# Kernel optimization log

Hardware: AMD Instinct MI355X
Metric: run time of the kernel (lower is better)

Reference implementation:

```python
import jax, jax.numpy as jnp
import numpy as np

N_NODES = 50000
N_EDGES = 1600000
IN_DIM = 128
HID = 64
HEADS = 4
N_GRAPHS = 64
OUT_DIM = 10
NEG_SLOPE = 0.2  # PyG GATConv default leaky_relu slope


def _glorot(key, shape):
    fan_in = shape[0] if len(shape) > 1 else shape[-1]
    return jax.random.normal(key, shape, dtype=jnp.float32) / np.sqrt(fan_in)


def setup_inputs() -> dict:
    key = jax.random.key(0)
    ks = jax.random.split(key, 24)
    imgs = jax.random.normal(ks[0], (N_NODES, IN_DIM), dtype=jnp.float32)
    edge_index = jax.random.randint(ks[1], (2, N_EDGES), 0, N_NODES, dtype=jnp.int32)
    batch = jnp.sort(jax.random.randint(ks[2], (N_NODES,), 0, N_GRAPHS, dtype=jnp.int32))
    HC = HID * HEADS
    inp = {
        'imgs': imgs, 'edge_index': edge_index, 'batch': batch,
        # superpixel aggregator: Linear(input_dim, hidden)
        'W_agg': _glorot(ks[3], (IN_DIM, HID)), 'b_agg': jnp.zeros((HID,), jnp.float32),
        # GAT layer 0: hidden -> heads*hidden, concat
        'W0': _glorot(ks[4], (HID, HC)), 'as0': _glorot(ks[5], (HEADS, HID)), 'ad0': _glorot(ks[6], (HEADS, HID)), 'b0': jnp.zeros((HC,), jnp.float32),
        # GAT layer 1: heads*hidden -> heads*hidden, concat
        'W1': _glorot(ks[7], (HC, HC)), 'as1': _glorot(ks[8], (HEADS, HID)), 'ad1': _glorot(ks[9], (HEADS, HID)), 'b1': jnp.zeros((HC,), jnp.float32),
        # GAT layer 2: heads*hidden -> hidden, mean over heads
        'W2': _glorot(ks[10], (HC, HC)), 'as2': _glorot(ks[11], (HEADS, HID)), 'ad2': _glorot(ks[12], (HEADS, HID)), 'b2': jnp.zeros((HID,), jnp.float32),
        # MLP: hidden -> hidden -> out
        'mW1': _glorot(ks[13], (HID, HID)), 'mb1': jnp.zeros((HID,), jnp.float32),
        'mW2': _glorot(ks[14], (HID, OUT_DIM)), 'mb2': jnp.zeros((OUT_DIM,), jnp.float32),
    }
    return inp


def _gat_conv(x, src, dst, W, a_src, a_dst, b, concat):
    # PyG GATConv: linear -> per-head scores -> leaky_relu -> segment softmax over dst -> scatter-add
    N = x.shape[0]
    H, C = a_src.shape
    h = (x @ W).reshape(N, H, C)                      # [N,H,C]
    es = jnp.sum(h * a_src, axis=-1)                  # [N,H]
    ed = jnp.sum(h * a_dst, axis=-1)                  # [N,H]
    e = jax.nn.leaky_relu(es[src] + ed[dst], NEG_SLOPE)  # [E,H]
    m = jax.ops.segment_max(e, dst, num_segments=N)
    m = jnp.where(jnp.isfinite(m), m, 0.0)
    ex = jnp.exp(e - m[dst])                          # [E,H]
    s = jax.ops.segment_sum(ex, dst, num_segments=N)
    alpha = ex / (s[dst] + 1e-16)                     # [E,H]
    out = jax.ops.segment_sum(h[src] * alpha[..., None], dst, num_segments=N)  # [N,H,C]
    out = out.reshape(N, H * C) if concat else out.mean(axis=1)
    return out + b


def _forward(imgs, edge_index, batch, W_agg, b_agg, W0, as0, ad0, b0, W1, as1, ad1, b1, W2, as2, ad2, b2, mW1, mb1, mW2, mb2):
    N = imgs.shape[0]
    # add self loops (PyG GATConv default add_self_loops=True)
    loop = jnp.arange(N, dtype=edge_index.dtype)
    src = jnp.concatenate([edge_index[0], loop])
    dst = jnp.concatenate([edge_index[1], loop])
    x = imgs @ W_agg + b_agg                          # lrgb aggregator
    x = jax.nn.elu(_gat_conv(x, src, dst, W0, as0, ad0, b0, True))
    x = jax.nn.elu(_gat_conv(x, src, dst, W1, as1, ad1, b1, True))
    x = _gat_conv(x, src, dst, W2, as2, ad2, b2, False)
    # global mean pool over graphs
    sums = jax.ops.segment_sum(x, batch, num_segments=N_GRAPHS)
    cnt = jax.ops.segment_sum(jnp.ones((N,), x.dtype), batch, num_segments=N_GRAPHS)
    pooled = sums / jnp.maximum(cnt, 1.0)[:, None]
    # MLP (dropout inactive at inference)
    hmlp = jax.nn.relu(pooled @ mW1 + mb1)
    return hmlp @ mW2 + mb2


def reference(imgs, edge_index, batch, W_agg, b_agg, W0, as0, ad0, b0, W1, as1, ad1, b1, W2, as2, ad2, b2, mW1, mb1, mW2, mb2):
    return _forward(imgs, edge_index, batch, W_agg, b_agg, W0, as0, ad0, b0, W1, as1, ad1, b1, W2, as2, ad2, b2, mW1, mb1, mW2, mb2)
```

## Files before the change

### kernel.cpp

```cpp
#include <hip/hip_runtime.h>
#include <hip/hip_bf16.h>

#define N_NODES 50000
#define N_EDGESX 1600000
#define E_TOT   (N_EDGESX + N_NODES)
#define IN_DIM 128
#define HID 64
#define HEADS 4
#define HC 256
#define N_GRAPHS 64
#define OUT_DIM 10
#define NEG_SLOPE 0.2f

#define NBUK 196
#define CAP 12288
#define BT 4096

typedef __attribute__((ext_vector_type(8))) short bf16x8;
typedef __attribute__((ext_vector_type(4))) float f32x4;

__device__ __forceinline__ float lrelu(float x){ return fmaxf(x, NEG_SLOPE*x); }
__device__ __forceinline__ float sel4(float4 v, int i){
  float r = v.x;
  r = (i==1) ? v.y : r;
  r = (i==2) ? v.z : r;
  r = (i==3) ? v.w : r;
  return r;
}
__device__ __forceinline__ unsigned short f2bf(float f){
  union { __hip_bfloat16 b; unsigned short u; } cv;
  cv.b = __float2bfloat16(f);
  return cv.u;
}
__device__ __forceinline__ float bflo(unsigned int u){ return __uint_as_float(u << 16); }
__device__ __forceinline__ float bfhi(unsigned int u){ return __uint_as_float(u & 0xffff0000u); }

__global__ __launch_bounds__(256) void bin_k(const int* __restrict__ ei,
                                             int* __restrict__ bucket_cursor,
                                             unsigned int* __restrict__ bucket_buf){
  __shared__ unsigned int pk[BT];
  __shared__ unsigned int binned[BT];
  __shared__ int hist[256], excl[256], gbase[256], lcur[256], tmp[256];
  const int tid = threadIdx.x;
  const int e0 = blockIdx.x * BT;
  const int nv = min(BT, E_TOT - e0);
  hist[tid] = 0;
  __syncthreads();
  for (int i = tid; i < nv; i += 256){
    int e = e0 + i;
    int src, dst;
    if (e < N_EDGESX){ src = ei[e]; dst = ei[N_EDGESX + e]; }
    else { src = e - N_EDGESX; dst = src; }
    pk[i] = ((unsigned)src << 16) | (unsigned)dst;
    atomicAdd(&hist[dst >> 8], 1);
  }
  __syncthreads();
  int v = hist[tid];
  tmp[tid] = v;
  __syncthreads();
  for (int off = 1; off < 256; off <<= 1){
    int t = (tid >= off) ? tmp[tid-off] : 0;
    __syncthreads();
    tmp[tid] += t;
    __syncthreads();
  }
  excl[tid] = tmp[tid] - v;
  lcur[tid] = tmp[tid] - v;
  if (tid < NBUK && v > 0) gbase[tid] = atomicAdd(&bucket_cursor[tid], v);
  __syncthreads();
  for (int i = tid; i < nv; i += 256){
    unsigned u = pk[i];
    int b = (int)((u & 0xFFFFu) >> 8);
    int p = atomicAdd(&lcur[b], 1);
    binned[p] = u;
  }
  __syncthreads();
  for (int j = tid; j < nv; j += 256){
    unsigned u = binned[j];
    int b = (int)((u & 0xFFFFu) >> 8);
    bucket_buf[(size_t)b*CAP + gbase[b] + (j - excl[b])] = u;
  }
}

__global__ __launch_bounds__(256) void bucket_scan_k(const int* __restrict__ bucket_cursor,
                                                     int* __restrict__ bucket_base,
                                                     int* __restrict__ row_start){
  __shared__ int tmp[256];
  int t = threadIdx.x;
  int v = (t < NBUK) ? bucket_cursor[t] : 0;
  tmp[t] = v;
  __syncthreads();
  for (int off = 1; off < 256; off <<= 1){
    int x = (t >= off) ? tmp[t-off] : 0;
    __syncthreads();
    tmp[t] += x;
    __syncthreads();
  }
  if (t < NBUK) bucket_base[t] = tmp[t] - v;
  if (t == 0) row_start[N_NODES] = E_TOT;
}

__global__ __launch_bounds__(256) void build_k(const unsigned int* __restrict__ bucket_buf,
                                               const int* __restrict__ bucket_cursor,
                                               const int* __restrict__ bucket_base,
                                               int* __restrict__ row_start,
                                               int* __restrict__ csr_src){
  __shared__ int hist[256], excl[256], lcur[256], tmp[256];
  const int b = blockIdx.x;
  const int t = threadIdx.x;
  const int cntb = bucket_cursor[b];
  const int base = bucket_base[b];
  const unsigned int* buf = bucket_buf + (size_t)b*CAP;
  hist[t] = 0;
  __syncthreads();
  for (int i = t; i < cntb; i += 256) atomicAdd(&hist[buf[i] & 255], 1);
  __syncthreads();
  int v = hist[t];
  tmp[t] = v;
  __syncthreads();
  for (int off = 1; off < 256; off <<= 1){
    int x = (t >= off) ? tmp[t-off] : 0;
    __syncthreads();
    tmp[t] += x;
    __syncthreads();
  }
  excl[t] = tmp[t] - v;
  lcur[t] = tmp[t] - v;
  int g = b*256 + t;
  if (g < N_NODES) row_start[g] = base + excl[t];
  __syncthreads();
  for (int i = t; i < cntb; i += 256){
    unsigned u = buf[i];
    int p = atomicAdd(&lcur[u & 255], 1);
    csr_src[base + p] = (int)(u >> 16);
  }
}

__global__ __launch_bounds__(256) void wcvt_k(const float* __restrict__ W, unsigned short* __restrict__ WT, int K){
  int idx = blockIdx.x*256 + threadIdx.x;
  if (idx >= K*256) return;
  int k = idx >> 8, c = idx & 255;
  WT[c*K + k] = f2bf(W[k*256 + c]);
}

__global__ __launch_bounds__(256) void agg_lin(const float* __restrict__ imgs, const float* __restrict__ W,
                                               const float* __restrict__ b, unsigned short* __restrict__ x0){
  __shared__ __align__(16) float xr[4][IN_DIM];
  int w = threadIdx.x >> 6, lane = threadIdx.x & 63;
  int n = blockIdx.x*4 + w;
  if (n >= N_NODES) return;
  ((float2*)xr[w])[lane] = ((const float2*)(imgs + (size_t)n*IN_DIM))[lane];
  float acc = b[lane];
  #pragma unroll 8
  for (int k = 0; k < IN_DIM; k++)
    acc = fmaf(xr[w][k], W[k*HID + lane], acc);
  x0[(size_t)n*HID + lane] = f2bf(acc);
}

template<int K>
__global__ __launch_bounds__(256) void lin_mfma(const unsigned short* __restrict__ x,
                                                const unsigned short* __restrict__ WT,
                                                const float* __restrict__ as_, const float* __restrict__ ad_,
                                                unsigned short* __restrict__ h,
                                                float* __restrict__ es, float* __restrict__ ed){
  constexpr int KP = K + 8;
  __shared__ __align__(16) unsigned short xs[16][KP];
  const int tid = threadIdx.x;
  const int lane = tid & 63;
  const int w = tid >> 6;
  const int n0 = blockIdx.x * 16;
  constexpr int CH = K/8;
  for (int i = tid; i < 16*CH; i += 256){
    int r = i / CH, cc = (i % CH)*8;
    *(uint4*)(&xs[r][cc]) = *(const uint4*)(x + (size_t)(n0+r)*K + cc);
  }
  __syncthreads();
  const int g  = lane >> 4;
  const int cl = lane & 15;
  f32x4 acc[4];
  #pragma unroll
  for (int c = 0; c < 4; c++) acc[c] = (f32x4){0.f,0.f,0.f,0.f};
  #pragma unroll
  for (int t = 0; t < K/32; t++){
    bf16x8 a = *(const bf16x8*)(&xs[cl][t*32 + g*8]);
    #pragma unroll
    for (int c = 0; c < 4; c++){
      bf16x8 bv = *(const bf16x8*)(WT + (size_t)(w*64 + c*16 + cl)*K + t*32 + g*8);
      acc[c] = __builtin_amdgcn_mfma_f32_16x16x32_bf16(a, bv, acc[c], 0, 0, 0);
    }
  }
  float pes[4] = {0.f,0.f,0.f,0.f}, ped[4] = {0.f,0.f,0.f,0.f};
  #pragma unroll
  for (int c = 0; c < 4; c++){
    float av = as_[w*64 + c*16 + cl];
    float dv = ad_[w*64 + c*16 + cl];
    #pragma unroll
    for (int j = 0; j < 4; j++){
      pes[j] = fmaf(acc[c][j], av, pes[j]);
      ped[j] = fmaf(acc[c][j], dv, ped[j]);
    }
  }
  #pragma unroll
  for (int off = 8; off >= 1; off >>= 1){
    #pragma unroll
    for (int j = 0; j < 4; j++){
      pes[j] += __shfl_xor(pes[j], off);
      ped[j] += __shfl_xor(ped[j], off);
    }
  }
  if (cl == 0){
    #pragma unroll
    for (int j = 0; j < 4; j++){
      int n = n0 + g*4 + j;
      es[n*4 + w] = pes[j];
      ed[n*4 + w] = ped[j];
    }
  }
  #pragma unroll
  for (int c = 0; c < 4; c++){
    #pragma unroll
    for (int j = 0; j < 4; j++){
      h[(size_t)(n0 + g*4 + j)*HC + w*64 + c*16 + cl] = f2bf(acc[c][j]);
    }
  }
}

template<int ACT, int OBF>
__global__ __launch_bounds__(256) void gat_agg(const unsigned short* __restrict__ h,
    const float* __restrict__ es, const float* __restrict__ ed,
    const int* __restrict__ row_start, const int* __restrict__ csr_src,
    const float* __restrict__ bias, void* __restrict__ outp){
  __shared__ int   sbuf[4][64];
  __shared__ float wbuf[4][64][4];
  const int lane = threadIdx.x & 63;
  const int wid  = threadIdx.x >> 6;
  const int n = blockIdx.x*4 + wid;
  if (n >= N_NODES) return;
  const int rs = row_start[n], re = row_start[n+1];
  const float4 edn = *(const float4*)(ed + n*4);
  const int half = lane >> 5;
  const int l5   = lane & 31;
  const int hh   = l5 >> 3;
  const unsigned voff_lane = (unsigned)(l5 << 3);

  float4 sum4 = make_float4(0.f,0.f,0.f,0.f);
  float a0=0.f,a1=0.f,a2=0.f,a3=0.f,a4=0.f,a5=0.f,a6=0.f,a7=0.f;

  for (int base = rs; base < re; base += 64){
    const int cl = min(64, re - base);
    int e = base + lane;
    int s = (e < re) ? csr_src[e] : 0;
    float4 e4 = *(const float4*)(es + (s<<2));
    float w0 = __expf(lrelu(e4.x + edn.x));
    float w1 = __expf(lrelu(e4.y + edn.y));
    float w2 = __expf(lrelu(e4.z + edn.z));
    float w3 = __expf(lrelu(e4.w + edn.w));
    if (e >= re){ w0=0.f; w1=0.f; w2=0.f; w3=0.f; }
    sum4.x += w0; sum4.y += w1; sum4.z += w2; sum4.w += w3;
    sbuf[wid][lane] = s;
    float4 wv4; wv4.x=w0; wv4.y=w1; wv4.z=w2; wv4.w=w3;
    *(float4*)wbuf[wid][lane] = wv4;
    for (int j = 0; j < cl; j += 2){
      int jj = j + half;
      float a  = wbuf[wid][jj][hh];
      int   s2 = sbuf[wid][jj];
      uint4 hv = *(const uint4*)(h + ((unsigned)(s2<<8) + voff_lane));
      a0 = fmaf(a, bflo(hv.x), a0);
      a1 = fmaf(a, bfhi(hv.x), a1);
      a2 = fmaf(a, bflo(hv.y), a2);
      a3 = fmaf(a, bfhi(hv.y), a3);
      a4 = fmaf(a, bflo(hv.z), a4);
      a5 = fmaf(a, bfhi(hv.z), a5);
      a6 = fmaf(a, bflo(hv.w), a6);
      a7 = fmaf(a, bfhi(hv.w), a7);
    }
  }
  #pragma unroll
  for (int off = 32; off >= 1; off >>= 1){
    sum4.x += __shfl_xor(sum4.x, off);
    sum4.y += __shfl_xor(sum4.y, off);
    sum4.z += __shfl_xor(sum4.z, off);
    sum4.w += __shfl_xor(sum4.w, off);
  }
  const float inv = 1.f / (sel4(sum4, hh) + 1e-16f);
  a0 += __shfl_xor(a0, 32); a1 += __shfl_xor(a1, 32);
  a2 += __shfl_xor(a2, 32); a3 += __shfl_xor(a3, 32);
  a4 += __shfl_xor(a4, 32); a5 += __shfl_xor(a5, 32);
  a6 += __shfl_xor(a6, 32); a7 += __shfl_xor(a7, 32);
  float4 o;
  o.x = (half ? a4 : a0) * inv;
  o.y = (half ? a5 : a1) * inv;
  o.z = (half ? a6 : a2) * inv;
  o.w = (half ? a7 : a3) * inv;
  const int fbase = l5*8 + half*4;
  if (ACT){
    float4 b4 = *(const float4*)(bias + fbase);
    o.x += b4.x; o.y += b4.y; o.z += b4.z; o.w += b4.w;
    o.x = o.x > 0.f ? o.x : expm1f(o.x);
    o.y = o.y > 0.f ? o.y : expm1f(o.y);
    o.z = o.z > 0.f ? o.z : expm1f(o.z);
    o.w = o.w > 0.f ? o.w : expm1f(o.w);
  }
  if (OBF){
    ushort4 ob;
    ob.x = f2bf(o.x); ob.y = f2bf(o.y); ob.z = f2bf(o.z); ob.w = f2bf(o.w);
    *(ushort4*)((unsigned short*)outp + (size_t)n*HC + fbase) = ob;
  } else {
    *(float4*)((float*)outp + (size_t)n*HC + fbase) = o;
  }
}

#define PB_NODES 128
__global__ __launch_bounds__(256) void pool_k(const float* __restrict__ xagg,
                                              const int* __restrict__ batch, float* __restrict__ pooled,
                                              float* __restrict__ cnt){
  int c = threadIdx.x & 63;
  int sub = threadIdx.x >> 6;
  int n0 = blockIdx.x * PB_NODES;
  int nend = n0 + PB_NODES; if (nend > N_NODES) nend = N_NODES;
  float acc = 0.f; int curg = -1; int cl = 0;
  for (int n = n0 + sub; n < nend; n += 4){
    int g = batch[n];
    if (g != curg){
      if (curg >= 0){
        unsafeAtomicAdd(pooled + curg*HID + c, acc);
        if (c == 0) unsafeAtomicAdd(cnt + curg, (float)cl);
      }
      curg = g; acc = 0.f; cl = 0;
    }
    const float* r = xagg + (size_t)n*HC;
    acc += 0.25f*(r[c] + r[64+c] + r[128+c] + r[192+c]);
    cl++;
  }
  if (curg >= 0){
    unsafeAtomicAdd(pooled + curg*HID + c, acc);
    if (c == 0) unsafeAtomicAdd(cnt + curg, (float)cl);
  }
}

__global__ __launch_bounds__(64) void mlp_k(const float* __restrict__ pooled, const float* __restrict__ cnt,
                                            const float* __restrict__ b2,
                                            const float* __restrict__ mW1, const float* __restrict__ mb1,
                                            const float* __restrict__ mW2, const float* __restrict__ mb2,
                                            float* __restrict__ out){
  __shared__ float p[HID], h1[HID];
  int g = blockIdx.x, j = threadIdx.x;
  float c = fmaxf(cnt[g], 1.f);
  p[j] = pooled[g*HID + j] / c + b2[j];
  __syncthreads();
  float acc = mb1[j];
  #pragma unroll 8
  for (int k = 0; k < HID; k++) acc = fmaf(p[k], mW1[k*HID + j], acc);
  h1[j] = fmaxf(acc, 0.f);
  __syncthreads();
  if (j < OUT_DIM){
    float a2 = mb2[j];
    #pragma unroll 8
    for (int k = 0; k < HID; k++) a2 = fmaf(h1[k], mW2[k*OUT_DIM + j], a2);
    out[g*OUT_DIM + j] = a2;
  }
}

extern "C" void kernel_launch(void* const* d_in, const int* in_sizes, int n_in,
                              void* d_out, int out_size, void* d_ws, size_t ws_size,
                              hipStream_t stream){
  const float* imgs  = (const float*)d_in[0];
  const int*   ei    = (const int*)d_in[1];
  const int*   batch = (const int*)d_in[2];
  const float* W_agg = (const float*)d_in[3];
  const float* b_agg = (const float*)d_in[4];
  const float* W0 = (const float*)d_in[5];
  const float* as0 = (const float*)d_in[6];
  const float* ad0 = (const float*)d_in[7];
  const float* b0 = (const float*)d_in[8];
  const float* W1 = (const float*)d_in[9];
  const float* as1 = (const float*)d_in[10];
  const float* ad1 = (const float*)d_in[11];
  const float* b1 = (const float*)d_in[12];
  const float* W2 = (const float*)d_in[13];
  const float* as2 = (const float*)d_in[14];
  const float* ad2 = (const float*)d_in[15];
  const float* b2 = (const float*)d_in[16];
  const float* mW1 = (const float*)d_in[17];
  const float* mb1 = (const float*)d_in[18];
  const float* mW2 = (const float*)d_in[19];
  const float* mb2 = (const float*)d_in[20];
  float* out = (float*)d_out;

  float* xf32 = (float*)d_ws;
  unsigned short* hb  = (unsigned short*)(xf32 + (size_t)N_NODES*HC);
  unsigned short* xbf = hb + (size_t)N_NODES*HC;
  float* es   = (float*)(xbf + (size_t)N_NODES*HC);
  float* ed   = es + (size_t)N_NODES*HEADS;
  float* pooled = ed + (size_t)N_NODES*HEADS;
  float* cnt  = pooled + N_GRAPHS*HID;
  int* row_start = (int*)(cnt + N_GRAPHS);
  int* csr_src   = row_start + (N_NODES+1);
  int* bucket_cursor = csr_src + E_TOT;
  int* bucket_base   = bucket_cursor + NBUK;
  unsigned short* WT0 = (unsigned short*)(bucket_base + NBUK);
  unsigned short* WT1 = WT0 + 256*64;
  unsigned short* WT2 = WT1 + 256*256;
  unsigned int* bucket_buf = (unsigned int*)(WT2 + 256*256);

  hipMemsetAsync(bucket_cursor, 0, NBUK*sizeof(int), stream);
  bin_k<<<(E_TOT + BT - 1)/BT, 256, 0, stream>>>(ei, bucket_cursor, bucket_buf);
  bucket_scan_k<<<1, 256, 0, stream>>>(bucket_cursor, bucket_base, row_start);
  build_k<<<NBUK, 256, 0, stream>>>(bucket_buf, bucket_cursor, bucket_base, row_start, csr_src);

  wcvt_k<<<(64*256+255)/256, 256, 0, stream>>>(W0, WT0, 64);
  wcvt_k<<<(256*256+255)/256, 256, 0, stream>>>(W1, WT1, 256);
  wcvt_k<<<(256*256+255)/256, 256, 0, stream>>>(W2, WT2, 256);

  agg_lin<<<(N_NODES+3)/4, 256, 0, stream>>>(imgs, W_agg, b_agg, xbf);

  const int MB = N_NODES/16;
  const int GB = (N_NODES + 3)/4;

  lin_mfma<64><<<MB, 256, 0, stream>>>(xbf, WT0, as0, ad0, hb, es, ed);
  gat_agg<1,1><<<GB, 256, 0, stream>>>(hb, es, ed, row_start, csr_src, b0, xbf);

  lin_mfma<256><<<MB, 256, 0, stream>>>(xbf, WT1, as1, ad1, hb, es, ed);
  gat_agg<1,1><<<GB, 256, 0, stream>>>(hb, es, ed, row_start, csr_src, b1, xbf);

  lin_mfma<256><<<MB, 256, 0, stream>>>(xbf, WT2, as2, ad2, hb, es, ed);
  gat_agg<0,0><<<GB, 256, 0, stream>>>(hb, es, ed, row_start, csr_src, nullptr, xf32);

  hipMemsetAsync(pooled, 0, (N_GRAPHS*HID + N_GRAPHS)*sizeof(float), stream);
  pool_k<<<(N_NODES + PB_NODES - 1)/PB_NODES, 256, 0, stream>>>(xf32, batch, pooled, cnt);
  mlp_k<<<N_GRAPHS, 64, 0, stream>>>(pooled, cnt, b2, mW1, mb1, mW2, mb2, out);
}
```

Measured before the change: 620.1 us.

## Aggregate before projecting in GAT layer 0 and split later aggregations per head

Layer 0 now computes attention scores straight from the 64-dim input through precomputed W0·a vectors. It aggregates the 64-dim features per head and only then applies the W0 projection, bias and ELU in a separate MFMA GEMM. This shrinks the per-edge gather from 256 to 64 bf16 values. Layers 1 and 2 store h in a head-major layout and launch one grid slice per head, which is meant to improve cache locality of the gathered rows, at the cost of recomputing the edge weights four times. Intermediate buffers reuse workspace regions such as bucket_buf and xf32.

```diff
diff --git a/kernel.cpp b/kernel.cpp
--- a/kernel.cpp
+++ b/kernel.cpp
@@ -143,8 +143,25 @@
   WT[c*K + k] = f2bf(W[k*256 + c]);
 }
 
+__global__ __launch_bounds__(256) void wproj_k(const float* __restrict__ W0,
+    const float* __restrict__ as0, const float* __restrict__ ad0,
+    float* __restrict__ ws0, float* __restrict__ wd0){
+  int t = threadIdx.x;
+  int h = t >> 6, k = t & 63;
+  float s = 0.f, d = 0.f;
+  for (int c = 0; c < 64; c++){
+    float wv = W0[k*256 + h*64 + c];
+    s = fmaf(wv, as0[h*64 + c], s);
+    d = fmaf(wv, ad0[h*64 + c], d);
+  }
+  ws0[t] = s; wd0[t] = d;
+}
+
 __global__ __launch_bounds__(256) void agg_lin(const float* __restrict__ imgs, const float* __restrict__ W,
-                                               const float* __restrict__ b, unsigned short* __restrict__ x0){
+                                               const float* __restrict__ b,
+                                               const float* __restrict__ ws0, const float* __restrict__ wd0,
+                                               unsigned short* __restrict__ x0,
+                                               float* __restrict__ es, float* __restrict__ ed){
   __shared__ __align__(16) float xr[4][IN_DIM];
   int w = threadIdx.x >> 6, lane = threadIdx.x & 63;
   int n = blockIdx.x*4 + w;
@@ -155,13 +172,150 @@
   for (int k = 0; k < IN_DIM; k++)
     acc = fmaf(xr[w][k], W[k*HID + lane], acc);
   x0[(size_t)n*HID + lane] = f2bf(acc);
+  float p[4], q[4];
+  #pragma unroll
+  for (int h = 0; h < 4; h++){
+    p[h] = acc * ws0[h*64 + lane];
+    q[h] = acc * wd0[h*64 + lane];
+  }
+  #pragma unroll
+  for (int off = 32; off >= 1; off >>= 1){
+    #pragma unroll
+    for (int h = 0; h < 4; h++){
+      p[h] += __shfl_xor(p[h], off);
+      q[h] += __shfl_xor(q[h], off);
+    }
+  }
+  if (lane == 0){
+    float4 pv; pv.x=p[0]; pv.y=p[1]; pv.z=p[2]; pv.w=p[3];
+    float4 qv; qv.x=q[0]; qv.y=q[1]; qv.z=q[2]; qv.w=q[3];
+    *(float4*)(es + n*4) = pv;
+    *(float4*)(ed + n*4) = qv;
+  }
+}
+
+__global__ __launch_bounds__(256) void gat_agg0(const unsigned short* __restrict__ x0,
+    const float* __restrict__ es, const float* __restrict__ ed,
+    const int* __restrict__ row_start, const int* __restrict__ csr_src,
+    unsigned short* __restrict__ y4){
+  __shared__ int   sbuf[4][64];
+  __shared__ float wbuf[4][64][4];
+  const int lane = threadIdx.x & 63;
+  const int wid  = threadIdx.x >> 6;
+  const int n = blockIdx.x*4 + wid;
+  if (n >= N_NODES) return;
+  const int rs = row_start[n], re = row_start[n+1];
+  const float4 edn = *(const float4*)(ed + n*4);
+  const int slot = lane >> 3;
+  const int f8   = lane & 7;
+  float4 sumw = make_float4(0.f,0.f,0.f,0.f);
+  float acc[4][8];
+  #pragma unroll
+  for (int h=0;h<4;h++)
+    #pragma unroll
+    for (int q2=0;q2<8;q2++) acc[h][q2]=0.f;
+
+  for (int base = rs; base < re; base += 64){
+    const int cl = min(64, re - base);
+    int e = base + lane;
+    int s = (e < re) ? csr_src[e] : 0;
+    float4 e4 = *(const float4*)(es + (s<<2));
+    float w0 = __expf(lrelu(e4.x + edn.x));
+    float w1 = __expf(lrelu(e4.y + edn.y));
+    float w2 = __expf(lrelu(e4.z + edn.z));
+    float w3 = __expf(lrelu(e4.w + edn.w));
+    if (e >= re){ w0=0.f; w1=0.f; w2=0.f; w3=0.f; }
+    sumw.x += w0; sumw.y += w1; sumw.z += w2; sumw.w += w3;
+    sbuf[wid][lane] = s;
+    float4 wv; wv.x=w0; wv.y=w1; wv.z=w2; wv.w=w3;
+    *(float4*)wbuf[wid][lane] = wv;
+    for (int j = 0; j < cl; j += 8){
+      int jj = j + slot;
+      if (jj < cl){
+        float4 aw = *(const float4*)wbuf[wid][jj];
+        int s2 = sbuf[wid][jj];
+        uint4 hv = *(const uint4*)(x0 + (((size_t)s2)<<6) + (f8<<3));
+        float f[8] = {bflo(hv.x),bfhi(hv.x),bflo(hv.y),bfhi(hv.y),
+                      bflo(hv.z),bfhi(hv.z),bflo(hv.w),bfhi(hv.w)};
+        #pragma unroll
+        for (int q2=0;q2<8;q2++){
+          acc[0][q2] = fmaf(aw.x, f[q2], acc[0][q2]);
+          acc[1][q2] = fmaf(aw.y, f[q2], acc[1][q2]);
+          acc[2][q2] = fmaf(aw.z, f[q2], acc[2][q2]);
+          acc[3][q2] = fmaf(aw.w, f[q2], acc[3][q2]);
+        }
+      }
+    }
+  }
+  #pragma unroll
+  for (int off = 8; off <= 32; off <<= 1){
+    #pragma unroll
+    for (int h=0;h<4;h++)
+      #pragma unroll
+      for (int q2=0;q2<8;q2++) acc[h][q2] += __shfl_xor(acc[h][q2], off);
+  }
+  #pragma unroll
+  for (int off = 32; off >= 1; off >>= 1){
+    sumw.x += __shfl_xor(sumw.x, off);
+    sumw.y += __shfl_xor(sumw.y, off);
+    sumw.z += __shfl_xor(sumw.z, off);
+    sumw.w += __shfl_xor(sumw.w, off);
+  }
+  if (lane < 32){
+    int h = lane >> 3;
+    float inv = 1.f / (sel4(sumw, h) + 1e-16f);
+    union { unsigned short u[8]; uint4 v; } ob;
+    #pragma unroll
+    for (int q2=0;q2<8;q2++) ob.u[q2] = f2bf(acc[h][q2] * inv);
+    *(uint4*)(y4 + (size_t)n*HC + lane*8) = ob.v;
+  }
+}
+
+__global__ __launch_bounds__(256) void hgemm_k(const unsigned short* __restrict__ y4,
+                                               const unsigned short* __restrict__ WT0,
+                                               const float* __restrict__ b0,
+                                               unsigned short* __restrict__ x1){
+  __shared__ __align__(16) unsigned short xs[16][264];
+  const int tid = threadIdx.x;
+  const int lane = tid & 63;
+  const int w = tid >> 6;
+  const int n0 = blockIdx.x * 16;
+  for (int i = tid; i < 16*32; i += 256){
+    int r = i >> 5, cc = (i & 31) * 8;
+    *(uint4*)(&xs[r][cc]) = *(const uint4*)(y4 + (size_t)(n0+r)*HC + cc);
+  }
+  __syncthreads();
+  const int g = lane >> 4, cl = lane & 15;
+  f32x4 acc[4];
+  #pragma unroll
+  for (int c = 0; c < 4; c++) acc[c] = (f32x4){0.f,0.f,0.f,0.f};
+  #pragma unroll
+  for (int t = 0; t < 2; t++){
+    bf16x8 a = *(const bf16x8*)(&xs[cl][w*64 + t*32 + g*8]);
+    #pragma unroll
+    for (int c = 0; c < 4; c++){
+      bf16x8 bv = *(const bf16x8*)(WT0 + (size_t)(w*64 + c*16 + cl)*64 + t*32 + g*8);
+      acc[c] = __builtin_amdgcn_mfma_f32_16x16x32_bf16(a, bv, acc[c], 0, 0, 0);
+    }
+  }
+  #pragma unroll
+  for (int c = 0; c < 4; c++){
+    int col = w*64 + c*16 + cl;
+    float bb = b0[col];
+    #pragma unroll
+    for (int j = 0; j < 4; j++){
+      float v = acc[c][j] + bb;
+      v = v > 0.f ? v : expm1f(v);
+      x1[(size_t)(n0 + g*4 + j)*HC + col] = f2bf(v);
+    }
+  }
 }
 
 template<int K>
 __global__ __launch_bounds__(256) void lin_mfma(const unsigned short* __restrict__ x,
                                                 const unsigned short* __restrict__ WT,
                                                 const float* __restrict__ as_, const float* __restrict__ ad_,
-                                                unsigned short* __restrict__ h,
+                                                unsigned short* __restrict__ hh,
                                                 float* __restrict__ es, float* __restrict__ ed){
   constexpr int KP = K + 8;
   __shared__ __align__(16) unsigned short xs[16][KP];
@@ -220,93 +374,89 @@
   for (int c = 0; c < 4; c++){
     #pragma unroll
     for (int j = 0; j < 4; j++){
-      h[(size_t)(n0 + g*4 + j)*HC + w*64 + c*16 + cl] = f2bf(acc[c][j]);
+      hh[((size_t)w*N_NODES + (n0 + g*4 + j))*HID + c*16 + cl] = f2bf(acc[c][j]);
     }
   }
 }
 
 template<int ACT, int OBF>
-__global__ __launch_bounds__(256) void gat_agg(const unsigned short* __restrict__ h,
+__global__ __launch_bounds__(256) void gat_agg_h(const unsigned short* __restrict__ hh,
     const float* __restrict__ es, const float* __restrict__ ed,
     const int* __restrict__ row_start, const int* __restrict__ csr_src,
     const float* __restrict__ bias, void* __restrict__ outp){
   __shared__ int   sbuf[4][64];
-  __shared__ float wbuf[4][64][4];
+  __shared__ float wbuf[4][64];
   const int lane = threadIdx.x & 63;
   const int wid  = threadIdx.x >> 6;
+  const int hy   = blockIdx.y;
   const int n = blockIdx.x*4 + wid;
   if (n >= N_NODES) return;
   const int rs = row_start[n], re = row_start[n+1];
-  const float4 edn = *(const float4*)(ed + n*4);
-  const int half = lane >> 5;
-  const int l5   = lane & 31;
-  const int hh   = l5 >> 3;
-  const unsigned voff_lane = (unsigned)(l5 << 3);
-
-  float4 sum4 = make_float4(0.f,0.f,0.f,0.f);
-  float a0=0.f,a1=0.f,a2=0.f,a3=0.f,a4=0.f,a5=0.f,a6=0.f,a7=0.f;
+  const float edh = ed[n*4 + hy];
+  const int slot = lane >> 3;
+  const int f8   = lane & 7;
+  const unsigned short* __restrict__ tab = hh + (((size_t)hy * N_NODES) << 6);
+  float sumw = 0.f;
+  float acc[8];
+  #pragma unroll
+  for (int q2=0;q2<8;q2++) acc[q2]=0.f;
 
   for (int base = rs; base < re; base += 64){
     const int cl = min(64, re - base);
     int e = base + lane;
     int s = (e < re) ? csr_src[e] : 0;
-    float4 e4 = *(const float4*)(es + (s<<2));
-    float w0 = __expf(lrelu(e4.x + edn.x));
-    float w1 = __expf(lrelu(e4.y + edn.y));
-    float w2 = __expf(lrelu(e4.z + edn.z));
-    float w3 = __expf(lrelu(e4.w + edn.w));
-    if (e >= re){ w0=0.f; w1=0.f; w2=0.f; w3=0.f; }
-    sum4.x += w0; sum4.y += w1; sum4.z += w2; sum4.w += w3;
+    float w = (e < re) ? __expf(lrelu(es[(s<<2)+hy] + edh)) : 0.f;
+    sumw += w;
     sbuf[wid][lane] = s;
-    float4 wv4; wv4.x=w0; wv4.y=w1; wv4.z=w2; wv4.w=w3;
-    *(float4*)wbuf[wid][lane] = wv4;
-    for (int j = 0; j < cl; j += 2){
-      int jj = j + half;
-      float a  = wbuf[wid][jj][hh];
-      int   s2 = sbuf[wid][jj];
-      uint4 hv = *(const uint4*)(h + ((unsigned)(s2<<8) + voff_lane));
-      a0 = fmaf(a, bflo(hv.x), a0);
-      a1 = fmaf(a, bfhi(hv.x), a1);
-      a2 = fmaf(a, bflo(hv.y), a2);
-      a3 = fmaf(a, bfhi(hv.y), a3);
-      a4 = fmaf(a, bflo(hv.z), a4);
-      a5 = fmaf(a, bfhi(hv.z), a5);
-      a6 = fmaf(a, bflo(hv.w), a6);
-      a7 = fmaf(a, bfhi(hv.w), a7);
-    }
-  }
-  #pragma unroll
-  for (int off = 32; off >= 1; off >>= 1){
-    sum4.x += __shfl_xor(sum4.x, off);
-    sum4.y += __shfl_xor(sum4.y, off);
-    sum4.z += __shfl_xor(sum4.z, off);
-    sum4.w += __shfl_xor(sum4.w, off);
-  }
-  const float inv = 1.f / (sel4(sum4, hh) + 1e-16f);
-  a0 += __shfl_xor(a0, 32); a1 += __shfl_xor(a1, 32);
-  a2 += __shfl_xor(a2, 32); a3 += __shfl_xor(a3, 32);
-  a4 += __shfl_xor(a4, 32); a5 += __shfl_xor(a5, 32);
-  a6 += __shfl_xor(a6, 32); a7 += __shfl_xor(a7, 32);
-  float4 o;
-  o.x = (half ? a4 : a0) * inv;
-  o.y = (half ? a5 : a1) * inv;
-  o.z = (half ? a6 : a2) * inv;
-  o.w = (half ? a7 : a3) * inv;
-  const int fbase = l5*8 + half*4;
+    wbuf[wid][lane] = w;
+    for (int j = 0; j < cl; j += 8){
+      int jj = j + slot;
+      if (jj < cl){
+        float a = wbuf[wid][jj];
+        int s2 = sbuf[wid][jj];
+        uint4 hv = *(const uint4*)(tab + (((size_t)s2)<<6) + (f8<<3));
+        acc[0] = fmaf(a, bflo(hv.x), acc[0]);
+        acc[1] = fmaf(a, bfhi(hv.x), acc[1]);
+        acc[2] = fmaf(a, bflo(hv.y), acc[2]);
+        acc[3] = fmaf(a, bfhi(hv.y), acc[3]);
+        acc[4] = fmaf(a, bflo(hv.z), acc[4]);
+        acc[5] = fmaf(a, bfhi(hv.z), acc[5]);
+        acc[6] = fmaf(a, bflo(hv.w), acc[6]);
+        acc[7] = fmaf(a, bfhi(hv.w), acc[7]);
+      }
+    }
+  }
+  #pragma unroll
+  for (int off = 8; off <= 32; off <<= 1){
+    #pragma unroll
+    for (int q2=0;q2<8;q2++) acc[q2] += __shfl_xor(acc[q2], off);
+  }
+  #pragma unroll
+  for (int off = 32; off >= 1; off >>= 1) sumw += __shfl_xor(sumw, off);
+  const float inv = 1.f / (sumw + 1e-16f);
+  float o[8];
+  #pragma unroll
+  for (int q2=0;q2<8;q2++) o[q2] = acc[q2]*inv;
   if (ACT){
-    float4 b4 = *(const float4*)(bias + fbase);
-    o.x += b4.x; o.y += b4.y; o.z += b4.z; o.w += b4.w;
-    o.x = o.x > 0.f ? o.x : expm1f(o.x);
-    o.y = o.y > 0.f ? o.y : expm1f(o.y);
-    o.z = o.z > 0.f ? o.z : expm1f(o.z);
-    o.w = o.w > 0.f ? o.w : expm1f(o.w);
-  }
-  if (OBF){
-    ushort4 ob;
-    ob.x = f2bf(o.x); ob.y = f2bf(o.y); ob.z = f2bf(o.z); ob.w = f2bf(o.w);
-    *(ushort4*)((unsigned short*)outp + (size_t)n*HC + fbase) = ob;
-  } else {
-    *(float4*)((float*)outp + (size_t)n*HC + fbase) = o;
+    #pragma unroll
+    for (int q2=0;q2<8;q2++){
+      float v = o[q2] + bias[hy*64 + f8*8 + q2];
+      o[q2] = v > 0.f ? v : expm1f(v);
+    }
+  }
+  if (lane < 8){
+    if (OBF){
+      union { unsigned short u[8]; uint4 v; } ob;
+      #pragma unroll
+      for (int q2=0;q2<8;q2++) ob.u[q2] = f2bf(o[q2]);
+      *(uint4*)((unsigned short*)outp + (size_t)n*HC + hy*64 + lane*8) = ob.v;
+    } else {
+      float* dst = (float*)outp + (size_t)n*HC + hy*64 + lane*8;
+      float4 v0; v0.x=o[0]; v0.y=o[1]; v0.z=o[2]; v0.w=o[3];
+      float4 v1; v1.x=o[4]; v1.y=o[5]; v1.z=o[6]; v1.w=o[7];
+      *(float4*)dst = v0;
+      *(float4*)(dst+4) = v1;
+    }
   }
 }
 
@@ -388,13 +538,16 @@
   float* out = (float*)d_out;
 
   float* xf32 = (float*)d_ws;
+  unsigned short* y4 = (unsigned short*)xf32;
   unsigned short* hb  = (unsigned short*)(xf32 + (size_t)N_NODES*HC);
   unsigned short* xbf = hb + (size_t)N_NODES*HC;
   float* es   = (float*)(xbf + (size_t)N_NODES*HC);
   float* ed   = es + (size_t)N_NODES*HEADS;
   float* pooled = ed + (size_t)N_NODES*HEADS;
   float* cnt  = pooled + N_GRAPHS*HID;
-  int* row_start = (int*)(cnt + N_GRAPHS);
+  float* ws0  = cnt + N_GRAPHS;
+  float* wd0  = ws0 + 256;
+  int* row_start = (int*)(wd0 + 256);
   int* csr_src   = row_start + (N_NODES+1);
   int* bucket_cursor = csr_src + E_TOT;
   int* bucket_base   = bucket_cursor + NBUK;
@@ -402,6 +555,7 @@
   unsigned short* WT1 = WT0 + 256*64;
   unsigned short* WT2 = WT1 + 256*256;
   unsigned int* bucket_buf = (unsigned int*)(WT2 + 256*256);
+  unsigned short* x0bf = (unsigned short*)bucket_buf;
 
   hipMemsetAsync(bucket_cursor, 0, NBUK*sizeof(int), stream);
   bin_k<<<(E_TOT + BT - 1)/BT, 256, 0, stream>>>(ei, bucket_cursor, bucket_buf);
@@ -411,20 +565,22 @@
   wcvt_k<<<(64*256+255)/256, 256, 0, stream>>>(W0, WT0, 64);
   wcvt_k<<<(256*256+255)/256, 256, 0, stream>>>(W1, WT1, 256);
   wcvt_k<<<(256*256+255)/256, 256, 0, stream>>>(W2, WT2, 256);
-
-  agg_lin<<<(N_NODES+3)/4, 256, 0, stream>>>(imgs, W_agg, b_agg, xbf);
+  wproj_k<<<1, 256, 0, stream>>>(W0, as0, ad0, ws0, wd0);
 
   const int MB = N_NODES/16;
   const int GB = (N_NODES + 3)/4;
-
-  lin_mfma<64><<<MB, 256, 0, stream>>>(xbf, WT0, as0, ad0, hb, es, ed);
-  gat_agg<1,1><<<GB, 256, 0, stream>>>(hb, es, ed, row_start, csr_src, b0, xbf);
+  dim3 GH(GB, HEADS, 1);
+
+  agg_lin<<<GB, 256, 0, stream>>>(imgs, W_agg, b_agg, ws0, wd0, x0bf, es, ed);
+
+  gat_agg0<<<GB, 256, 0, stream>>>(x0bf, es, ed, row_start, csr_src, y4);
+  hgemm_k<<<MB, 256, 0, stream>>>(y4, WT0, b0, xbf);
 
   lin_mfma<256><<<MB, 256, 0, stream>>>(xbf, WT1, as1, ad1, hb, es, ed);
-  gat_agg<1,1><<<GB, 256, 0, stream>>>(hb, es, ed, row_start, csr_src, b1, xbf);
+  gat_agg_h<1,1><<<GH, 256, 0, stream>>>(hb, es, ed, row_start, csr_src, b1, xbf);
 
   lin_mfma<256><<<MB, 256, 0, stream>>>(xbf, WT2, as2, ad2, hb, es, ed);
-  gat_agg<0,0><<<GB, 256, 0, stream>>>(hb, es, ed, row_start, csr_src, nullptr, xf32);
+  gat_agg_h<0,0><<<GH, 256, 0, stream>>>(hb, es, ed, row_start, csr_src, nullptr, xf32);
 
   hipMemsetAsync(pooled, 0, (N_GRAPHS*HID + N_GRAPHS)*sizeof(float), stream);
   pool_k<<<(N_NODES + PB_NODES - 1)/PB_NODES, 256, 0, stream>>>(xf32, batch, pooled, cnt);
```

Result: slower. 678.1 us (+9.3%).
